# Optimization experiments

Hardware: AMD Instinct MI355X
Metric: run time of the kernel (lower is better)

## Reference

```python
import jax, jax.numpy as jnp
import numpy as np

B = 128            # number of subgraphs (one head, one tail each)
NODES_PER_G = 64
N = B * NODES_PER_G  # 8192 total nodes
E = 131072           # total edges in the batched graph
NUM_RELS = 200
D = 64               # rel_emb_dim
EMB = 64             # emb_dim
L = 3                # num_gcn_layers (jumping-knowledge concat)
REPR = L * EMB       # 192, g.ndata['repr'] feature width
LINK_MODE = 6


def setup_inputs() -> dict:
    key = jax.random.key(0)
    ks = jax.random.split(key, 10)
    node_repr = jax.random.normal(ks[0], (N, REPR), jnp.float32)
    edge_src = jax.random.randint(ks[1], (E,), 0, N, dtype=jnp.int32)
    edge_dst = jax.random.randint(ks[2], (E,), 0, N, dtype=jnp.int32)
    edge_type = jax.random.randint(ks[3], (E,), 0, NUM_RELS, dtype=jnp.int32)
    rel_labels = jax.random.randint(ks[4], (B,), 0, NUM_RELS, dtype=jnp.int32)
    node_graph_id = (jnp.arange(N) // NODES_PER_G).astype(jnp.int32)
    head_ids = (jnp.arange(B) * NODES_PER_G).astype(jnp.int32)   # node with id==1 per graph
    tail_ids = head_ids + 1                                      # node with id==2 per graph
    rel_emb_w = jax.random.normal(ks[5], (NUM_RELS, D), jnp.float32)
    W_reld = jax.random.normal(ks[6], (LINK_MODE, D, D), jnp.float32) * 0.05
    b_reld = jnp.zeros((LINK_MODE, D), jnp.float32)
    Wc = jax.random.normal(ks[7], (D, 2 * D), jnp.float32) * 0.05
    bc = jnp.zeros((D,), jnp.float32)
    Wf = jax.random.normal(ks[8], (1, 3 * REPR + D), jnp.float32) * 0.05
    bf = jnp.zeros((1,), jnp.float32)
    return {
        'node_repr': node_repr, 'rel_emb_w': rel_emb_w, 'W_reld': W_reld,
        'b_reld': b_reld, 'Wc': Wc, 'bc': bc, 'Wf': Wf, 'bf': bf,
        'edge_src': edge_src, 'edge_dst': edge_dst, 'edge_type': edge_type,
        'rel_labels': rel_labels, 'node_graph_id': node_graph_id,
        'head_ids': head_ids, 'tail_ids': tail_ids,
    }


def reference(node_repr, rel_emb_w, W_reld, b_reld, Wc, bc, Wf, bf,
              edge_src, edge_dst, edge_type, rel_labels, node_graph_id,
              head_ids, tail_ids):
    f32 = jnp.float32
    nb = head_ids.shape[0]
    # Six edge connection modes, [B, E] each (row b selects edges incident to
    # the head/tail node of subgraph b).
    io = (edge_dst[None, :] == head_ids[:, None]).astype(f32)  # in_edge_out
    oo = (edge_src[None, :] == head_ids[:, None]).astype(f32)  # out_edge_out
    ii = (edge_dst[None, :] == tail_ids[:, None]).astype(f32)  # in_edge_in
    oi = (edge_src[None, :] == tail_ids[:, None]).astype(f32)  # out_edge_in
    m5 = oo * ii   # edge_mode_5: head -> tail edges
    m6 = io * oi   # edge_mode_6: tail -> head edges
    modes = jnp.stack([io - m6, oo - m5, ii - m5, oi - m6, m5, m6])  # [6,B,E]
    norms = modes.sum(-1, keepdims=True) + 1e-30                      # [6,B,1]
    # Per-mode linear transform of relation embeddings, then aggregate.
    rel_feat = rel_emb_w[edge_type]                                   # [E,D]
    trans = jnp.einsum('ed,mfd->mef', rel_feat, W_reld) + b_reld[:, None, :]  # [6,E,D]
    contrib = jnp.einsum('mbe,med->mbd', modes, trans) / norms        # [6,B,D]
    rel_neighbor = contrib.mean(0)                                    # sum(...)/link_mode
    rel_final = jnp.concatenate([rel_neighbor, rel_emb_w[rel_labels]], -1) @ Wc.T + bc
    rel_final = jax.nn.relu(rel_final)
    rel_final = rel_final / jnp.maximum(
        jnp.linalg.norm(rel_final, axis=-1, keepdims=True), 1e-12)
    # mean_nodes(g, 'repr') per subgraph
    g_sum = jax.ops.segment_sum(node_repr, node_graph_id, num_segments=nb)
    counts = jax.ops.segment_sum(jnp.ones((node_repr.shape[0],), f32),
                                 node_graph_id, num_segments=nb)
    g_out = g_sum / counts[:, None]
    g_rep = jnp.concatenate(
        [g_out, node_repr[head_ids], node_repr[tail_ids], rel_final], -1)
    return g_rep @ Wf.T + bf   # [B, 1]
```

## Files before the change

### kernel.cpp

```cpp
#include <hip/hip_runtime.h>

#define NGRAPH 128
#define NEDGE  131072
#define DIM    64
#define REPRW  192
#define NTHREADS 1024
#define MAXHITS 1024

__global__ __launch_bounds__(NTHREADS) void fused_graph_kernel(
    const float* __restrict__ node_repr, const float* __restrict__ rel_emb,
    const float* __restrict__ W_reld, const float* __restrict__ b_reld,
    const float* __restrict__ Wc, const float* __restrict__ bc,
    const float* __restrict__ Wf, const float* __restrict__ bf,
    const int* __restrict__ esrc, const int* __restrict__ edst,
    const int* __restrict__ etype, const int* __restrict__ rel_labels,
    const int* __restrict__ head_ids, const int* __restrict__ tail_ids,
    float* __restrict__ out)
{
    const int b    = blockIdx.x;
    const int tid  = threadIdx.x;
    const int base = b << 6;
    const int wave = tid >> 6;
    const int lane = tid & 63;

    __shared__ __align__(16) float shS[6 * 64];
    __shared__ float shCnt[6];
    __shared__ int   shList[MAXHITS];
    __shared__ int   shNHits;
    __shared__ float sh_grep[640];
    __shared__ float sh_part[4 * 192];
    __shared__ float sh_v[6 * 64];
    __shared__ float sh_rn[64];
    __shared__ float sh_Wc[64 * 129];
    __shared__ float sh_red[16];

    if (tid < 384) shS[tid] = 0.0f;
    if (tid < 6)   shCnt[tid] = 0.0f;
    if (tid == 0)  shNHits = 0;
    __syncthreads();

    {
        int r = tid / 192, col = tid - r * 192;
        if (tid < 768) {
            const float* p = node_repr + (size_t)(base + r * 16) * REPRW + col;
            float a = 0.0f;
            #pragma unroll
            for (int n = 0; n < 16; n++) a += p[(size_t)n * REPRW];
            sh_part[r * 192 + col] = a;
        }
        if (tid < 192) {
            sh_grep[192 + tid] = node_repr[(size_t)head_ids[b] * REPRW + tid];
            sh_grep[384 + tid] = node_repr[(size_t)tail_ids[b] * REPRW + tid];
        }
    }

    {
        const int4* s4 = (const int4*)esrc;
        const int4* d4 = (const int4*)edst;
        for (int i = tid; i < NEDGE / 4; i += NTHREADS) {
            int4 ss = s4[i];
            int4 dd = d4[i];
            #pragma unroll
            for (int c = 0; c < 4; c++) {
                int s = (c == 0) ? ss.x : (c == 1) ? ss.y : (c == 2) ? ss.z : ss.w;
                int d = (c == 0) ? dd.x : (c == 1) ? dd.y : (c == 2) ? dd.z : dd.w;
                bool hd = (unsigned)(d - base) < 2u;
                bool hs = (unsigned)(s - base) < 2u;
                if (hd | hs) {
                    int et = etype[4 * i + c];
                    if (hd) {
                        if (d == base) {
                            int m = (s == base + 1) ? 5 : 0;
                            int idx = atomicAdd(&shNHits, 1);
                            if (idx < MAXHITS) shList[idx] = (m << 16) | et;
                            atomicAdd(&shCnt[m], 1.0f);
                        } else if (s != base) {
                            int idx = atomicAdd(&shNHits, 1);
                            if (idx < MAXHITS) shList[idx] = (2 << 16) | et;
                            atomicAdd(&shCnt[2], 1.0f);
                        }
                    }
                    if (hs) {
                        if (s == base) {
                            int m = (d == base + 1) ? 4 : 1;
                            int idx = atomicAdd(&shNHits, 1);
                            if (idx < MAXHITS) shList[idx] = (m << 16) | et;
                            atomicAdd(&shCnt[m], 1.0f);
                        } else if (d != base) {
                            int idx = atomicAdd(&shNHits, 1);
                            if (idx < MAXHITS) shList[idx] = (3 << 16) | et;
                            atomicAdd(&shCnt[3], 1.0f);
                        }
                    }
                }
            }
        }
    }
    __syncthreads();

    {
        int nh = shNHits < MAXHITS ? shNHits : MAXHITS;
        for (int h = wave; h < nh; h += 16) {
            int ent = shList[h];
            int m = ent >> 16, t = ent & 0xffff;
            atomicAdd(&shS[m * 64 + lane], rel_emb[t * 64 + lane]);
        }
        if (tid < 192)
            sh_grep[tid] = (sh_part[tid] + sh_part[192 + tid] +
                            sh_part[384 + tid] + sh_part[576 + tid]) * (1.0f / 64.0f);
    }
    __syncthreads();

    if (tid < 384) {
        int m = wave, f = lane;
        const float4* Wrow = (const float4*)(W_reld + (m * 64 + f) * 64);
        const float4* Sv   = (const float4*)(shS + m * 64);
        float dot = 0.0f;
        #pragma unroll
        for (int k = 0; k < 16; k++) {
            float4 w = Wrow[k];
            float4 sv = Sv[k];
            dot += w.x * sv.x + w.y * sv.y + w.z * sv.z + w.w * sv.w;
        }
        float cm = shCnt[m];
        sh_v[m * 64 + f] = (dot + cm * b_reld[m * 64 + f]) / (cm + 1e-30f);
    } else {
        for (int j = tid - 384; j < 64 * 128; j += NTHREADS - 384) {
            int row = j >> 7, col = j & 127;
            sh_Wc[row * 129 + col] = Wc[j];
        }
    }
    __syncthreads();

    if (tid < 64) {
        sh_rn[tid] = (sh_v[tid] + sh_v[64 + tid] + sh_v[128 + tid] +
                      sh_v[192 + tid] + sh_v[256 + tid] + sh_v[320 + tid]) * (1.0f / 6.0f);
    }
    __syncthreads();

    if (tid < 64) {
        const float* rl = rel_emb + rel_labels[b] * DIM;
        const float* Wrow = sh_Wc + tid * 129;
        float z = bc[tid];
        #pragma unroll 8
        for (int j = 0; j < 64; j++) z += sh_rn[j] * Wrow[j];
        #pragma unroll 8
        for (int j = 0; j < 64; j++) z += rl[j] * Wrow[64 + j];
        z = fmaxf(z, 0.0f);
        float sq = z * z;
        #pragma unroll
        for (int off = 32; off >= 1; off >>= 1) sq += __shfl_xor(sq, off);
        float nrm = fmaxf(sqrtf(sq), 1e-12f);
        sh_grep[576 + tid] = z / nrm;
    }
    __syncthreads();

    if (tid < 640) {
        float p = sh_grep[tid] * Wf[tid];
        #pragma unroll
        for (int off = 32; off >= 1; off >>= 1) p += __shfl_xor(p, off);
        if (lane == 0) sh_red[wave] = p;
    }
    __syncthreads();
    if (tid == 0) {
        float acc = bf[0];
        #pragma unroll
        for (int w = 0; w < 10; w++) acc += sh_red[w];
        out[b] = acc;
    }
}

extern "C" void kernel_launch(void* const* d_in, const int* in_sizes, int n_in,
                              void* d_out, int out_size, void* d_ws, size_t ws_size,
                              hipStream_t stream) {
    (void)in_sizes; (void)n_in; (void)out_size; (void)d_ws; (void)ws_size;

    const float* node_repr = (const float*)d_in[0];
    const float* rel_emb   = (const float*)d_in[1];
    const float* W_reld    = (const float*)d_in[2];
    const float* b_reld    = (const float*)d_in[3];
    const float* Wc        = (const float*)d_in[4];
    const float* bc        = (const float*)d_in[5];
    const float* Wf        = (const float*)d_in[6];
    const float* bf        = (const float*)d_in[7];
    const int*   esrc      = (const int*)d_in[8];
    const int*   edst      = (const int*)d_in[9];
    const int*   etype     = (const int*)d_in[10];
    const int*   rel_labels= (const int*)d_in[11];
    const int*   head_ids  = (const int*)d_in[13];
    const int*   tail_ids  = (const int*)d_in[14];

    fused_graph_kernel<<<NGRAPH, NTHREADS, 0, stream>>>(
        node_repr, rel_emb, W_reld, b_reld, Wc, bc, Wf, bf,
        esrc, edst, etype, rel_labels, head_ids, tail_ids, (float*)d_out);
}
```

Measured before the change: 113.1 us.

## Split edge scan into a single global pass binning hits per graph

Replaces the per-block full scan of all edges with one grid-wide scan kernel that classifies each edge once and appends mode/type entries to per-graph lists in workspace via global atomics. The finish kernel then reads only its own list to accumulate relation embeddings and mode counts. This removes the redundant reading of the edge arrays by every block, at the cost of an extra memset, a second launch and global atomics.

Result: slower. 118.4 us (+4.7%).

```diff
diff --git a/kernel.cpp b/kernel.cpp
--- a/kernel.cpp
+++ b/kernel.cpp
@@ -4,17 +4,57 @@
 #define NEDGE  131072
 #define DIM    64
 #define REPRW  192
-#define NTHREADS 1024
-#define MAXHITS 1024
-
-__global__ __launch_bounds__(NTHREADS) void fused_graph_kernel(
+#define LISTCAP 1024
+
+
+__global__ __launch_bounds__(256) void edge_scan_kernel(
+    const int* __restrict__ esrc, const int* __restrict__ edst,
+    const int* __restrict__ etype, int* __restrict__ gcnt,
+    int* __restrict__ glist)
+{
+    const int i = blockIdx.x * 256 + threadIdx.x;
+    const int4 ss = ((const int4*)esrc)[i];
+    const int4 dd = ((const int4*)edst)[i];
+    #pragma unroll
+    for (int c = 0; c < 4; c++) {
+        const int s = (c == 0) ? ss.x : (c == 1) ? ss.y : (c == 2) ? ss.z : ss.w;
+        const int d = (c == 0) ? dd.x : (c == 1) ? dd.y : (c == 2) ? dd.z : dd.w;
+        const bool hs = (s & 63) < 2;
+        const bool hd = (d & 63) < 2;
+        if (hd | hs) {
+            const int et = etype[4 * i + c];
+            if (hd) {
+                const int g = d >> 6, gb = g << 6;
+                int m = -1;
+                if (d == gb)       m = (s == gb + 1) ? 5 : 0;
+                else if (s != gb)  m = 2;
+                if (m >= 0) {
+                    int slot = atomicAdd(&gcnt[g], 1);
+                    if (slot < LISTCAP) glist[g * LISTCAP + slot] = (m << 8) | et;
+                }
+            }
+            if (hs) {
+                const int g = s >> 6, gb = g << 6;
+                int m = -1;
+                if (s == gb)       m = (d == gb + 1) ? 4 : 1;
+                else if (d != gb)  m = 3;
+                if (m >= 0) {
+                    int slot = atomicAdd(&gcnt[g], 1);
+                    if (slot < LISTCAP) glist[g * LISTCAP + slot] = (m << 8) | et;
+                }
+            }
+        }
+    }
+}
+
+__global__ __launch_bounds__(1024) void graph_finish_kernel(
     const float* __restrict__ node_repr, const float* __restrict__ rel_emb,
     const float* __restrict__ W_reld, const float* __restrict__ b_reld,
     const float* __restrict__ Wc, const float* __restrict__ bc,
     const float* __restrict__ Wf, const float* __restrict__ bf,
-    const int* __restrict__ esrc, const int* __restrict__ edst,
-    const int* __restrict__ etype, const int* __restrict__ rel_labels,
+    const int* __restrict__ rel_labels,
     const int* __restrict__ head_ids, const int* __restrict__ tail_ids,
+    const int* __restrict__ gcnt, const int* __restrict__ glist,
     float* __restrict__ out)
 {
     const int b    = blockIdx.x;
@@ -25,8 +65,7 @@
 
     __shared__ __align__(16) float shS[6 * 64];
     __shared__ float shCnt[6];
-    __shared__ int   shList[MAXHITS];
-    __shared__ int   shNHits;
+    __shared__ int   shNH;
     __shared__ float sh_grep[640];
     __shared__ float sh_part[4 * 192];
     __shared__ float sh_v[6 * 64];
@@ -36,9 +75,22 @@
 
     if (tid < 384) shS[tid] = 0.0f;
     if (tid < 6)   shCnt[tid] = 0.0f;
-    if (tid == 0)  shNHits = 0;
-    __syncthreads();
-
+    if (tid == 0) {
+        int n = gcnt[b];
+        shNH = n < LISTCAP ? n : LISTCAP;
+    }
+    __syncthreads();
+
+    {
+        const int nh = shNH;
+        const int* mylist = glist + b * LISTCAP;
+        for (int h = wave; h < nh; h += 16) {
+            int ent = mylist[h];
+            int m = ent >> 8, t = ent & 0xff;
+            atomicAdd(&shS[m * 64 + lane], rel_emb[t * 64 + lane]);
+            if (lane == 0) atomicAdd(&shCnt[m], 1.0f);
+        }
+    }
     {
         int r = tid / 192, col = tid - r * 192;
         if (tid < 768) {
@@ -53,62 +105,6 @@
             sh_grep[384 + tid] = node_repr[(size_t)tail_ids[b] * REPRW + tid];
         }
     }
-
-    {
-        const int4* s4 = (const int4*)esrc;
-        const int4* d4 = (const int4*)edst;
-        for (int i = tid; i < NEDGE / 4; i += NTHREADS) {
-            int4 ss = s4[i];
-            int4 dd = d4[i];
-            #pragma unroll
-            for (int c = 0; c < 4; c++) {
-                int s = (c == 0) ? ss.x : (c == 1) ? ss.y : (c == 2) ? ss.z : ss.w;
-                int d = (c == 0) ? dd.x : (c == 1) ? dd.y : (c == 2) ? dd.z : dd.w;
-                bool hd = (unsigned)(d - base) < 2u;
-                bool hs = (unsigned)(s - base) < 2u;
-                if (hd | hs) {
-                    int et = etype[4 * i + c];
-                    if (hd) {
-                        if (d == base) {
-                            int m = (s == base + 1) ? 5 : 0;
-                            int idx = atomicAdd(&shNHits, 1);
-                            if (idx < MAXHITS) shList[idx] = (m << 16) | et;
-                            atomicAdd(&shCnt[m], 1.0f);
-                        } else if (s != base) {
-                            int idx = atomicAdd(&shNHits, 1);
-                            if (idx < MAXHITS) shList[idx] = (2 << 16) | et;
-                            atomicAdd(&shCnt[2], 1.0f);
-                        }
-                    }
-                    if (hs) {
-                        if (s == base) {
-                            int m = (d == base + 1) ? 4 : 1;
-                            int idx = atomicAdd(&shNHits, 1);
-                            if (idx < MAXHITS) shList[idx] = (m << 16) | et;
-                            atomicAdd(&shCnt[m], 1.0f);
-                        } else if (d != base) {
-                            int idx = atomicAdd(&shNHits, 1);
-                            if (idx < MAXHITS) shList[idx] = (3 << 16) | et;
-                            atomicAdd(&shCnt[3], 1.0f);
-                        }
-                    }
-                }
-            }
-        }
-    }
-    __syncthreads();
-
-    {
-        int nh = shNHits < MAXHITS ? shNHits : MAXHITS;
-        for (int h = wave; h < nh; h += 16) {
-            int ent = shList[h];
-            int m = ent >> 16, t = ent & 0xffff;
-            atomicAdd(&shS[m * 64 + lane], rel_emb[t * 64 + lane]);
-        }
-        if (tid < 192)
-            sh_grep[tid] = (sh_part[tid] + sh_part[192 + tid] +
-                            sh_part[384 + tid] + sh_part[576 + tid]) * (1.0f / 64.0f);
-    }
     __syncthreads();
 
     if (tid < 384) {
@@ -125,7 +121,7 @@
         float cm = shCnt[m];
         sh_v[m * 64 + f] = (dot + cm * b_reld[m * 64 + f]) / (cm + 1e-30f);
     } else {
-        for (int j = tid - 384; j < 64 * 128; j += NTHREADS - 384) {
+        for (int j = tid - 384; j < 64 * 128; j += 1024 - 384) {
             int row = j >> 7, col = j & 127;
             sh_Wc[row * 129 + col] = Wc[j];
         }
@@ -135,6 +131,10 @@
     if (tid < 64) {
         sh_rn[tid] = (sh_v[tid] + sh_v[64 + tid] + sh_v[128 + tid] +
                       sh_v[192 + tid] + sh_v[256 + tid] + sh_v[320 + tid]) * (1.0f / 6.0f);
+    } else if (tid >= 128 && tid < 320) {
+        int j = tid - 128;
+        sh_grep[j] = (sh_part[j] + sh_part[192 + j] +
+                      sh_part[384 + j] + sh_part[576 + j]) * (1.0f / 64.0f);
     }
     __syncthreads();
 
@@ -173,7 +173,7 @@
 extern "C" void kernel_launch(void* const* d_in, const int* in_sizes, int n_in,
                               void* d_out, int out_size, void* d_ws, size_t ws_size,
                               hipStream_t stream) {
-    (void)in_sizes; (void)n_in; (void)out_size; (void)d_ws; (void)ws_size;
+    (void)in_sizes; (void)n_in; (void)out_size; (void)ws_size;
 
     const float* node_repr = (const float*)d_in[0];
     const float* rel_emb   = (const float*)d_in[1];
@@ -190,7 +190,13 @@
     const int*   head_ids  = (const int*)d_in[13];
     const int*   tail_ids  = (const int*)d_in[14];
 
-    fused_graph_kernel<<<NGRAPH, NTHREADS, 0, stream>>>(
+    int* gcnt  = (int*)d_ws;
+    int* glist = (int*)((char*)d_ws + 512);
+
+    hipMemsetAsync(gcnt, 0, NGRAPH * sizeof(int), stream);
+    edge_scan_kernel<<<NEDGE / 4 / 256, 256, 0, stream>>>(
+        esrc, edst, etype, gcnt, glist);
+    graph_finish_kernel<<<NGRAPH, 1024, 0, stream>>>(
         node_repr, rel_emb, W_reld, b_reld, Wc, bc, Wf, bf,
-        esrc, edst, etype, rel_labels, head_ids, tail_ids, (float*)d_out);
+        rel_labels, head_ids, tail_ids, gcnt, glist, (float*)d_out);
 }
```
